# Optimization experiments

Measured on AMD Instinct MI355X. Metric: run time of the kernel, lower is better.

The kernel has to match this reference:

```python
import jax, jax.numpy as jnp
import numpy as np

N, E, F, R, S = 20000, 320000, 64, 8, 10
AVG_NEIGH = 16.0


def setup_inputs() -> dict:
    key = jax.random.key(0)
    ks = jax.random.split(key, 16)
    inp = {
        "vectors": jax.random.normal(ks[0], (E, 3), jnp.float32),
        "node_feats": jax.random.normal(ks[1], (N, F, 4), jnp.float32),  # [N, F, 1(0e)+3(1o)]
        "node_specie": jax.random.randint(ks[2], (N,), 0, S),
        "radial_embedding": jax.random.normal(ks[3], (E, R), jnp.float32),
        "senders": jax.random.randint(ks[4], (E,), 0, N),
        "receivers": jax.random.randint(ks[5], (E,), 0, N),
        # residual FullyConnectedTensorProduct(feats, one-hot species 0e) == species-dep. linear per l
        "W_res_s": jax.random.normal(ks[6], (S, F, F), jnp.float32),
        "W_res_v": jax.random.normal(ks[7], (S, F, F), jnp.float32),
        # interaction block: input linear per l
        "W_in_s": jax.random.normal(ks[8], (F, F), jnp.float32),
        "W_in_v": jax.random.normal(ks[9], (F, F), jnp.float32),
        # radial MLP -> 5 CG tensor-product path weights per channel
        "mlp_w1": jax.random.normal(ks[10], (R, 64), jnp.float32),
        "mlp_w2": jax.random.normal(ks[11], (64, 5 * F), jnp.float32) / 8.0,
        # interaction block: output linear per l
        "W_out_s": jax.random.normal(ks[12], (F, F), jnp.float32),
        "W_out_v": jax.random.normal(ks[13], (F, F), jnp.float32),
        # symmetric product basis (correlation 3), species-dependent term weights
        "W_prod_s": jax.random.normal(ks[14], (S, 5, F), jnp.float32) * 0.3,
        "W_prod_v": jax.random.normal(ks[15], (S, 4, F), jnp.float32) * 0.3,
    }
    k2 = jax.random.split(jax.random.key(1), 3)
    inp["W_lin_s"] = jax.random.normal(k2[0], (F, F), jnp.float32)
    inp["W_lin_v"] = jax.random.normal(k2[1], (F, F), jnp.float32)
    inp["W_read"] = jax.random.normal(k2[2], (F, 1), jnp.float32)
    return inp


def _forward(vectors, node_feats, node_specie, radial_embedding, senders, receivers,
             W_res_s, W_res_v, W_in_s, W_in_v, mlp_w1, mlp_w2, W_out_s, W_out_v,
             W_prod_s, W_prod_v, W_lin_s, W_lin_v, W_read):
    inv_sf = 1.0 / jnp.sqrt(jnp.float32(F))
    s = node_feats[..., 0]          # [N,F]   0e channels
    v = node_feats[..., 1:]         # [N,F,3] 1o channels

    # --- residual connection: FCTP(feats, one-hot species 0e attrs) -> species-gated linear per l
    res_s = jnp.einsum('nf,ngf->ng', s, W_res_s[node_specie]) * inv_sf
    res_v = jnp.einsum('nfc,ngf->ngc', v, W_res_v[node_specie]) * inv_sf

    # --- InteractionBlock ---
    h_s = (s @ W_in_s) * inv_sf
    h_v = jnp.einsum('nfc,fg->ngc', v, W_in_v) * inv_sf

    # spherical harmonics up to max_ell=1: Y0 = 1, Y1 = unit edge vector
    r = jnp.sqrt(jnp.sum(vectors * vectors, -1) + 1e-12)
    Y1 = vectors / r[:, None]                                # [E,3]

    # radial MLP produces per-edge weights for the 5 CG paths:
    # (0e x Y0 -> 0e), (1o . Y1 -> 0e), (0e x Y1 -> 1o), (1o x Y0 -> 1o), (1o x Y1 -> 1o, cross)
    w = (jax.nn.silu(radial_embedding @ mlp_w1) @ mlp_w2).reshape(-1, 5, F)  # [E,5,F]

    ss = h_s[senders]                                        # [E,F]
    sv = h_v[senders]                                        # [E,F,3]
    dot = jnp.einsum('efc,ec->ef', sv, Y1)                   # [E,F]
    m_s = w[:, 0] * ss + w[:, 1] * dot                       # [E,F]
    m_v = (w[:, 2] * ss)[:, :, None] * Y1[:, None, :] \
        + w[:, 3][:, :, None] * sv \
        + w[:, 4][:, :, None] * jnp.cross(sv, Y1[:, None, :])  # [E,F,3]

    agg_s = jnp.zeros_like(h_s).at[receivers].add(m_s) / AVG_NEIGH
    agg_v = jnp.zeros_like(h_v).at[receivers].add(m_v) / AVG_NEIGH
    a_s = (agg_s @ W_out_s) * inv_sf
    a_v = jnp.einsum('nfc,fg->ngc', agg_v, W_out_v) * inv_sf

    # --- EquivariantProductBasisBlock: correlation-3 symmetric contraction, species-dependent ---
    vv = jnp.sum(a_v * a_v, -1)                              # [N,F] invariant |v|^2
    Wp = W_prod_s[node_specie]                               # [N,5,F]
    p_s = (Wp[:, 0] * a_s + Wp[:, 1] * a_s ** 2 + Wp[:, 2] * a_s ** 3
           + Wp[:, 3] * vv + Wp[:, 4] * a_s * vv)
    Wv = W_prod_v[node_specie]                               # [N,4,F]
    p_v = (Wv[:, 0] + Wv[:, 1] * a_s + Wv[:, 2] * a_s ** 2 + Wv[:, 3] * vv)[:, :, None] * a_v

    f_s = (p_s @ W_lin_s) * inv_sf + res_s
    f_v = jnp.einsum('nfc,fg->ngc', p_v, W_lin_v) * inv_sf + res_v

    # --- LinearReadoutBlock (output_irreps = 0e), 1 head ---
    node_out = ((f_s @ W_read) * inv_sf)[:, None, :]         # [N, heads=1, 1]
    new_feats = jnp.concatenate([f_s[..., None], f_v], axis=-1)  # [N,F,4]
    return node_out, new_feats


def reference(vectors, node_feats, node_specie, radial_embedding, senders, receivers,
              W_res_s, W_res_v, W_in_s, W_in_v, mlp_w1, mlp_w2, W_out_s, W_out_v,
              W_prod_s, W_prod_v, W_lin_s, W_lin_v, W_read):
    return _forward(vectors, node_feats, node_specie, radial_embedding, senders, receivers,
                    W_res_s, W_res_v, W_in_s, W_in_v, mlp_w1, mlp_w2, W_out_s, W_out_v,
                    W_prod_s, W_prod_v, W_lin_s, W_lin_v, W_read)
```

## Files before the change

kernel.cpp:

```cpp
#include <hip/hip_runtime.h>
#include <math.h>

#define NN 20000
#define NE 320000
#define NF (NN*64)
#define TB 16

__global__ __launch_bounds__(256) void k_transpose_res(
    const float* __restrict__ Ws, const float* __restrict__ Wv,
    float* __restrict__ Wst, float* __restrict__ Wvt)
{
  int i = blockIdx.x*256 + threadIdx.x;
  int spec = i >> 12;
  int g = (i >> 6) & 63;
  int f = i & 63;
  Wst[spec*4096 + f*64 + g] = Ws[i];
  Wvt[spec*4096 + f*64 + g] = Wv[i];
}

__global__ __launch_bounds__(256) void k_hist_rank(const int* __restrict__ receivers,
                                                   int* __restrict__ count,
                                                   int* __restrict__ rank)
{
  int e = blockIdx.x*256 + threadIdx.x;
  rank[e] = atomicAdd(&count[receivers[e]], 1);
}

__global__ __launch_bounds__(256) void k_scan(const int* __restrict__ count,
                                              int* __restrict__ offset)
{
  __shared__ int part[256];
  int t = threadIdx.x;
  const int PER = 79;
  int s = 0;
  for(int i=0;i<PER;++i){ int idx = t*PER+i; if(idx < NN) s += count[idx]; }
  part[t] = s;
  __syncthreads();
  for(int off=1; off<256; off<<=1){
    int v = (t>=off) ? part[t-off] : 0;
    __syncthreads();
    part[t] += v;
    __syncthreads();
  }
  int run = t ? part[t-1] : 0;
  for(int i=0;i<PER;++i){
    int idx = t*PER+i;
    if(idx < NN){ offset[idx] = run; run += count[idx]; }
  }
  if(t==255) offset[NN] = run;
}

__global__ __launch_bounds__(256) void k_scatter(
    const int* __restrict__ senders, const int* __restrict__ receivers,
    const float* __restrict__ vectors, const float* __restrict__ radial,
    const int* __restrict__ offset, const int* __restrict__ rank,
    int* __restrict__ srt_snd, int* __restrict__ srt_rcv,
    float* __restrict__ srt_y, float* __restrict__ srt_rad)
{
  int e = blockIdx.x*256 + threadIdx.x;
  int r = receivers[e];
  int slot = offset[r] + rank[e];
  srt_snd[slot] = senders[e];
  srt_rcv[slot] = r;
  float vx = vectors[e*3], vy = vectors[e*3+1], vz = vectors[e*3+2];
  float rinv = rsqrtf(vx*vx + vy*vy + vz*vz + 1e-12f);
  float4 y4; y4.x = vx*rinv; y4.y = vy*rinv; y4.z = vz*rinv; y4.w = 0.f;
  *(float4*)(srt_y + (size_t)slot*4) = y4;
  float4 ra = *(const float4*)(radial + (size_t)e*8);
  float4 rb = *(const float4*)(radial + (size_t)e*8 + 4);
  *(float4*)(srt_rad + (size_t)slot*8)     = ra;
  *(float4*)(srt_rad + (size_t)slot*8 + 4) = rb;
}

__global__ __launch_bounds__(256) void k_node_pre(
    const float* __restrict__ node_feats, const float* __restrict__ W_in_s,
    const float* __restrict__ W_in_v, float* __restrict__ h)
{
  __shared__ float sh[16][4][64];
  int wave = threadIdx.x >> 6, lane = threadIdx.x & 63;
  int nb = blockIdx.x*16 + wave*4;
  #pragma unroll
  for(int k=0;k<4;++k){
    int nd = wave*4 + k;
    float4 nf = *(const float4*)(node_feats + (size_t)((nb+k)*64 + lane)*4);
    sh[nd][0][lane]=nf.x; sh[nd][1][lane]=nf.y; sh[nd][2][lane]=nf.z; sh[nd][3][lane]=nf.w;
  }
  __syncthreads();
  float as[4]={0,0,0,0}, a0[4]={0,0,0,0}, a1[4]={0,0,0,0}, a2[4]={0,0,0,0};
  for(int f=0; f<64; ++f){
    float ws = W_in_s[f*64+lane], wv = W_in_v[f*64+lane];
    #pragma unroll
    for(int k=0;k<4;++k){
      int nd = wave*4 + k;
      as[k] = fmaf(sh[nd][0][f], ws, as[k]);
      a0[k] = fmaf(sh[nd][1][f], wv, a0[k]);
      a1[k] = fmaf(sh[nd][2][f], wv, a1[k]);
      a2[k] = fmaf(sh[nd][3][f], wv, a2[k]);
    }
  }
  #pragma unroll
  for(int k=0;k<4;++k){
    float4 o4; o4.x = as[k]*0.125f; o4.y = a0[k]*0.125f;
    o4.z = a1[k]*0.125f; o4.w = a2[k]*0.125f;
    *(float4*)(h + (size_t)((nb+k)*64 + lane)*4) = o4;
  }
}

__global__ __launch_bounds__(256) void k_edge(
    const float* __restrict__ srt_y, const float* __restrict__ srt_rad,
    const int* __restrict__ srt_snd, const int* __restrict__ srt_rcv,
    const float* __restrict__ mlp_w1, const float* __restrict__ mlp_w2,
    const float* __restrict__ h, float* __restrict__ agg)
{
  __shared__ int   sndS[4][TB];
  __shared__ int   rcvS[4][TB];
  __shared__ float yS[4][4*TB];
  __shared__ float rad[4][8*TB];
  __shared__ float hid[4][TB][64];
  int wave = threadIdx.x >> 6, lane = threadIdx.x & 63;
  int e0 = (blockIdx.x*4 + wave)*TB;

  if(lane < TB){
    sndS[wave][lane] = srt_snd[e0 + lane];
    rcvS[wave][lane] = srt_rcv[e0 + lane];
  }
  yS[wave][lane]     = srt_y[(size_t)e0*4 + lane];
  rad[wave][lane]    = srt_rad[(size_t)e0*8 + lane];
  rad[wave][64+lane] = srt_rad[(size_t)e0*8 + 64 + lane];
  float wl[8];
  #pragma unroll
  for(int r=0;r<8;++r) wl[r] = mlp_w1[r*64+lane];

  #pragma unroll
  for(int t=0;t<TB;++t){
    float acc = 0.f;
    #pragma unroll
    for(int r=0;r<8;++r) acc = fmaf(rad[wave][t*8+r], wl[r], acc);
    hid[wave][t][lane] = acc / (1.f + __expf(-acc));
  }

  float w[5][TB];
  #pragma unroll
  for(int j=0;j<5;++j)
    #pragma unroll
    for(int t=0;t<TB;++t) w[j][t] = 0.f;
  for(int hh=0; hh<64; hh+=2){
    float b0[5], b1[5];
    #pragma unroll
    for(int j=0;j<5;++j){
      b0[j] = mlp_w2[hh*320     + j*64 + lane];
      b1[j] = mlp_w2[(hh+1)*320 + j*64 + lane];
    }
    #pragma unroll
    for(int t=0;t<TB;++t){
      float2 hb = *(const float2*)&hid[wave][t][hh];
      #pragma unroll
      for(int j=0;j<5;++j) w[j][t] = fmaf(hb.x, b0[j], fmaf(hb.y, b1[j], w[j][t]));
    }
  }

  float4 hv[4];
  #pragma unroll
  for(int p=0;p<4;++p)
    hv[p] = *(const float4*)(h + (size_t)(sndS[wave][p]*64 + lane)*4);

  float as_=0.f, av0=0.f, av1=0.f, av2=0.f;
  int cur = rcvS[wave][0];
  #pragma unroll
  for(int t=0;t<TB;++t){
    float4 hc = hv[t&3];
    if(t+4 < TB)
      hv[t&3] = *(const float4*)(h + (size_t)(sndS[wave][t+4]*64 + lane)*4);
    int rcv = rcvS[wave][t];
    if(rcv != cur){
      size_t ro = (size_t)(cur*64 + lane)*4;
      atomicAdd(&agg[ro],   as_);
      atomicAdd(&agg[ro+1], av0);
      atomicAdd(&agg[ro+2], av1);
      atomicAdd(&agg[ro+3], av2);
      as_=0.f; av0=0.f; av1=0.f; av2=0.f;
      cur = rcv;
    }
    float y0=yS[wave][t*4], y1=yS[wave][t*4+1], y2=yS[wave][t*4+2];
    float ss=hc.x, sv0=hc.y, sv1=hc.z, sv2=hc.w;
    float dot = sv0*y0 + sv1*y1 + sv2*y2;
    as_ += w[0][t]*ss + w[1][t]*dot;
    float w2s = w[2][t]*ss, w3t = w[3][t], w4t = w[4][t];
    av0 += w2s*y0 + w3t*sv0 + w4t*(sv1*y2 - sv2*y1);
    av1 += w2s*y1 + w3t*sv1 + w4t*(sv2*y0 - sv0*y2);
    av2 += w2s*y2 + w3t*sv2 + w4t*(sv0*y1 - sv1*y0);
  }
  size_t ro = (size_t)(cur*64 + lane)*4;
  atomicAdd(&agg[ro],   as_);
  atomicAdd(&agg[ro+1], av0);
  atomicAdd(&agg[ro+2], av1);
  atomicAdd(&agg[ro+3], av2);
}

__global__ __launch_bounds__(256) void k_node_post(
  const float* __restrict__ node_feats, const int* __restrict__ specie,
  const float* __restrict__ agg,
  const float* __restrict__ Wrst, const float* __restrict__ Wrvt,
  const float* __restrict__ W_out_s, const float* __restrict__ W_out_v,
  const float* __restrict__ W_prod_s, const float* __restrict__ W_prod_v,
  const float* __restrict__ W_lin_s, const float* __restrict__ W_lin_v,
  const float* __restrict__ W_read, float* __restrict__ out_node,
  float* __restrict__ out_feats)
{
  __shared__ float shA[16][4][64];
  __shared__ float shS[16][4][64];
  int wave = threadIdx.x >> 6, lane = threadIdx.x & 63;
  int nb = blockIdx.x*16 + wave*4;
  #pragma unroll
  for(int k=0;k<4;++k){
    int nd = wave*4 + k;
    float4 ag = *(const float4*)(agg + (size_t)((nb+k)*64 + lane)*4);
    shA[nd][0][lane] = ag.x * (1.f/16.f);
    shA[nd][1][lane] = ag.y * (1.f/16.f);
    shA[nd][2][lane] = ag.z * (1.f/16.f);
    shA[nd][3][lane] = ag.w * (1.f/16.f);
    float4 nf = *(const float4*)(node_feats + (size_t)((nb+k)*64 + lane)*4);
    shS[nd][0][lane]=nf.x; shS[nd][1][lane]=nf.y; shS[nd][2][lane]=nf.z; shS[nd][3][lane]=nf.w;
  }
  int spec[4];
  #pragma unroll
  for(int k=0;k<4;++k) spec[k] = specie[nb+k];
  __syncthreads();
  float a_s[4]={0,0,0,0}, a0[4]={0,0,0,0}, a1[4]={0,0,0,0}, a2[4]={0,0,0,0};
  float r_s[4]={0,0,0,0}, r0[4]={0,0,0,0}, r1[4]={0,0,0,0}, r2[4]={0,0,0,0};
  for(int f=0; f<64; ++f){
    float wos = W_out_s[f*64+lane], wov = W_out_v[f*64+lane];
    #pragma unroll
    for(int k=0;k<4;++k){
      int nd = wave*4 + k;
      a_s[k] = fmaf(shA[nd][0][f], wos, a_s[k]);
      a0[k]  = fmaf(shA[nd][1][f], wov, a0[k]);
      a1[k]  = fmaf(shA[nd][2][f], wov, a1[k]);
      a2[k]  = fmaf(shA[nd][3][f], wov, a2[k]);
    }
    #pragma unroll
    for(int k=0;k<4;++k){
      int nd = wave*4 + k;
      float wrs = Wrst[spec[k]*4096 + f*64 + lane];
      float wrv = Wrvt[spec[k]*4096 + f*64 + lane];
      r_s[k] = fmaf(shS[nd][0][f], wrs, r_s[k]);
      r0[k]  = fmaf(shS[nd][1][f], wrv, r0[k]);
      r1[k]  = fmaf(shS[nd][2][f], wrv, r1[k]);
      r2[k]  = fmaf(shS[nd][3][f], wrv, r2[k]);
    }
  }
  __syncthreads();
  #pragma unroll
  for(int k=0;k<4;++k){
    int nd = wave*4 + k;
    float A_s = a_s[k]*0.125f, A0 = a0[k]*0.125f, A1 = a1[k]*0.125f, A2 = a2[k]*0.125f;
    float vv = A0*A0 + A1*A1 + A2*A2;
    float as2 = A_s*A_s;
    const float* Wp = W_prod_s + spec[k]*320;
    float p_s = Wp[lane]*A_s + Wp[64+lane]*as2 + Wp[128+lane]*as2*A_s
              + Wp[192+lane]*vv + Wp[256+lane]*A_s*vv;
    const float* Wq = W_prod_v + spec[k]*256;
    float coef = Wq[lane] + Wq[64+lane]*A_s + Wq[128+lane]*as2 + Wq[192+lane]*vv;
    shS[nd][0][lane] = p_s;
    shS[nd][1][lane] = coef*A0;
    shS[nd][2][lane] = coef*A1;
    shS[nd][3][lane] = coef*A2;
  }
  __syncthreads();
  float lfs[4]={0,0,0,0}, lf0[4]={0,0,0,0}, lf1[4]={0,0,0,0}, lf2[4]={0,0,0,0};
  for(int f=0; f<64; ++f){
    float wls = W_lin_s[f*64+lane], wlv = W_lin_v[f*64+lane];
    #pragma unroll
    for(int k=0;k<4;++k){
      int nd = wave*4 + k;
      lfs[k] = fmaf(shS[nd][0][f], wls, lfs[k]);
      lf0[k] = fmaf(shS[nd][1][f], wlv, lf0[k]);
      lf1[k] = fmaf(shS[nd][2][f], wlv, lf1[k]);
      lf2[k] = fmaf(shS[nd][3][f], wlv, lf2[k]);
    }
  }
  float wr = W_read[lane];
  #pragma unroll
  for(int k=0;k<4;++k){
    int n = nb + k;
    float FS = lfs[k]*0.125f + r_s[k]*0.125f;
    float F0 = lf0[k]*0.125f + r0[k]*0.125f;
    float F1 = lf1[k]*0.125f + r1[k]*0.125f;
    float F2 = lf2[k]*0.125f + r2[k]*0.125f;
    float x = FS * wr;
    #pragma unroll
    for(int off=32; off; off>>=1) x += __shfl_down(x, off);
    if(lane==0) out_node[n] = x*0.125f;
    float4 o4; o4.x=FS; o4.y=F0; o4.z=F1; o4.w=F2;
    *(float4*)(out_feats + (size_t)(n*64+lane)*4) = o4;
  }
}

extern "C" void kernel_launch(void* const* d_in, const int* in_sizes, int n_in,
                              void* d_out, int out_size, void* d_ws, size_t ws_size,
                              hipStream_t stream) {
  const float* vectors    = (const float*)d_in[0];
  const float* node_feats = (const float*)d_in[1];
  const int*   node_specie= (const int*)  d_in[2];
  const float* radial     = (const float*)d_in[3];
  const int*   senders    = (const int*)  d_in[4];
  const int*   receivers  = (const int*)  d_in[5];
  const float* W_res_s    = (const float*)d_in[6];
  const float* W_res_v    = (const float*)d_in[7];
  const float* W_in_s     = (const float*)d_in[8];
  const float* W_in_v     = (const float*)d_in[9];
  const float* mlp_w1     = (const float*)d_in[10];
  const float* mlp_w2     = (const float*)d_in[11];
  const float* W_out_s    = (const float*)d_in[12];
  const float* W_out_v    = (const float*)d_in[13];
  const float* W_prod_s   = (const float*)d_in[14];
  const float* W_prod_v   = (const float*)d_in[15];
  const float* W_lin_s    = (const float*)d_in[16];
  const float* W_lin_v    = (const float*)d_in[17];
  const float* W_read     = (const float*)d_in[18];

  float* ws   = (float*)d_ws;
  float* h    = ws;
  float* agg  = ws + 4*(size_t)NF;
  float* Wrst = ws + 8*(size_t)NF;
  float* Wrvt = Wrst + 40960;
  float* srt_rad = Wrvt + 40960;
  float* srt_y   = srt_rad + 8*(size_t)NE;
  int*   srt_snd = (int*)(srt_y + 4*(size_t)NE);
  int*   srt_rcv = srt_snd + NE;
  int*   rank    = srt_rcv + NE;
  int*   offset  = rank + NE;
  int*   count   = offset + NN + 1;

  hipMemsetAsync(agg,   0, (size_t)4*NF*sizeof(float), stream);
  hipMemsetAsync(count, 0, (size_t)NN*sizeof(int), stream);
  k_transpose_res<<<160, 256, 0, stream>>>(W_res_s, W_res_v, Wrst, Wrvt);
  k_hist_rank<<<NE/256, 256, 0, stream>>>(receivers, count, rank);
  k_scan     <<<1,      256, 0, stream>>>(count, offset);
  k_scatter  <<<NE/256, 256, 0, stream>>>(senders, receivers, vectors, radial,
                                          offset, rank, srt_snd, srt_rcv, srt_y, srt_rad);
  k_node_pre<<<NN/16, 256, 0, stream>>>(node_feats, W_in_s, W_in_v, h);
  k_edge<<<NE/(4*TB), 256, 0, stream>>>(srt_y, srt_rad, srt_snd, srt_rcv,
                                        mlp_w1, mlp_w2, h, agg);
  k_node_post<<<NN/16, 256, 0, stream>>>(node_feats, node_specie, agg,
                                         Wrst, Wrvt, W_out_s, W_out_v,
                                         W_prod_s, W_prod_v, W_lin_s, W_lin_v,
                                         W_read, (float*)d_out, (float*)d_out + NN);
}
```

Before: 536.7 us.

## Pack sorted edge data into 64-byte records and use packed FMA for radial MLP

The scatter kernel now writes each sorted edge as one 16-float record (unit vector, sender, radial features, receiver). The edge kernel loads that record with a single coalesced float4 per lane, replacing four separate arrays and their loads. The hid shared buffer is transposed so the 64x320 MLP layer can use packed two-wide FMAs over pairs of edges. The agg buffer also moves to a planar per-node layout, so atomics and the k_node_post loads touch contiguous 64-lane runs; the cost is a padded record that writes extra bytes in the scatter pass.

```diff
diff --git a/kernel.cpp b/kernel.cpp
--- a/kernel.cpp
+++ b/kernel.cpp
@@ -5,6 +5,16 @@
 #define NE 320000
 #define NF (NN*64)
 #define TB 16
+
+typedef float v2f __attribute__((ext_vector_type(2)));
+
+#if __has_builtin(__builtin_elementwise_fma)
+#define PKFMA(a,b,c) __builtin_elementwise_fma(a,b,c)
+#else
+static __device__ __forceinline__ v2f PKFMA(v2f a, v2f b, v2f c){
+  v2f r; r.x = fmaf(a.x,b.x,c.x); r.y = fmaf(a.y,b.y,c.y); return r;
+}
+#endif
 
 __global__ __launch_bounds__(256) void k_transpose_res(
     const float* __restrict__ Ws, const float* __restrict__ Wv,
@@ -54,22 +64,22 @@
     const int* __restrict__ senders, const int* __restrict__ receivers,
     const float* __restrict__ vectors, const float* __restrict__ radial,
     const int* __restrict__ offset, const int* __restrict__ rank,
-    int* __restrict__ srt_snd, int* __restrict__ srt_rcv,
-    float* __restrict__ srt_y, float* __restrict__ srt_rad)
+    float* __restrict__ rec)
 {
   int e = blockIdx.x*256 + threadIdx.x;
   int r = receivers[e];
   int slot = offset[r] + rank[e];
-  srt_snd[slot] = senders[e];
-  srt_rcv[slot] = r;
   float vx = vectors[e*3], vy = vectors[e*3+1], vz = vectors[e*3+2];
   float rinv = rsqrtf(vx*vx + vy*vy + vz*vz + 1e-12f);
-  float4 y4; y4.x = vx*rinv; y4.y = vy*rinv; y4.z = vz*rinv; y4.w = 0.f;
-  *(float4*)(srt_y + (size_t)slot*4) = y4;
   float4 ra = *(const float4*)(radial + (size_t)e*8);
   float4 rb = *(const float4*)(radial + (size_t)e*8 + 4);
-  *(float4*)(srt_rad + (size_t)slot*8)     = ra;
-  *(float4*)(srt_rad + (size_t)slot*8 + 4) = rb;
+  float* rp = rec + (size_t)slot*16;
+  float4 w0; w0.x = vx*rinv; w0.y = vy*rinv; w0.z = vz*rinv; w0.w = __int_as_float(senders[e]);
+  float4 w3; w3.x = __int_as_float(r); w3.y = 0.f; w3.z = 0.f; w3.w = 0.f;
+  *(float4*)(rp)      = w0;
+  *(float4*)(rp + 4)  = ra;
+  *(float4*)(rp + 8)  = rb;
+  *(float4*)(rp + 12) = w3;
 }
 
 __global__ __launch_bounds__(256) void k_node_pre(
@@ -107,26 +117,17 @@
 }
 
 __global__ __launch_bounds__(256) void k_edge(
-    const float* __restrict__ srt_y, const float* __restrict__ srt_rad,
-    const int* __restrict__ srt_snd, const int* __restrict__ srt_rcv,
+    const float* __restrict__ rec,
     const float* __restrict__ mlp_w1, const float* __restrict__ mlp_w2,
     const float* __restrict__ h, float* __restrict__ agg)
 {
-  __shared__ int   sndS[4][TB];
-  __shared__ int   rcvS[4][TB];
-  __shared__ float yS[4][4*TB];
-  __shared__ float rad[4][8*TB];
-  __shared__ float hid[4][TB][64];
+  __shared__ float recS[4][256];
+  __shared__ float hid[4][64][20];
   int wave = threadIdx.x >> 6, lane = threadIdx.x & 63;
   int e0 = (blockIdx.x*4 + wave)*TB;
 
-  if(lane < TB){
-    sndS[wave][lane] = srt_snd[e0 + lane];
-    rcvS[wave][lane] = srt_rcv[e0 + lane];
-  }
-  yS[wave][lane]     = srt_y[(size_t)e0*4 + lane];
-  rad[wave][lane]    = srt_rad[(size_t)e0*8 + lane];
-  rad[wave][64+lane] = srt_rad[(size_t)e0*8 + 64 + lane];
+  *(float4*)&recS[wave][lane*4] = *(const float4*)(rec + (size_t)e0*16 + lane*4);
+
   float wl[8];
   #pragma unroll
   for(int r=0;r<8;++r) wl[r] = mlp_w1[r*64+lane];
@@ -135,66 +136,73 @@
   for(int t=0;t<TB;++t){
     float acc = 0.f;
     #pragma unroll
-    for(int r=0;r<8;++r) acc = fmaf(rad[wave][t*8+r], wl[r], acc);
-    hid[wave][t][lane] = acc / (1.f + __expf(-acc));
-  }
-
-  float w[5][TB];
+    for(int r=0;r<8;++r) acc = fmaf(recS[wave][t*16+4+r], wl[r], acc);
+    hid[wave][lane][t] = acc / (1.f + __expf(-acc));
+  }
+
+  v2f wv[5][8];
   #pragma unroll
   for(int j=0;j<5;++j)
     #pragma unroll
-    for(int t=0;t<TB;++t) w[j][t] = 0.f;
-  for(int hh=0; hh<64; hh+=2){
-    float b0[5], b1[5];
+    for(int tp=0;tp<8;++tp) wv[j][tp] = (v2f){0.f, 0.f};
+  const float* w2p = mlp_w2 + lane;
+  for(int hh=0; hh<64; ++hh){
+    float b[5];
+    #pragma unroll
+    for(int j=0;j<5;++j) b[j] = w2p[hh*320 + j*64];
+    v2f hv[8];
+    #pragma unroll
+    for(int tp=0;tp<8;++tp) hv[tp] = *(const v2f*)&hid[wave][hh][2*tp];
     #pragma unroll
     for(int j=0;j<5;++j){
-      b0[j] = mlp_w2[hh*320     + j*64 + lane];
-      b1[j] = mlp_w2[(hh+1)*320 + j*64 + lane];
-    }
-    #pragma unroll
-    for(int t=0;t<TB;++t){
-      float2 hb = *(const float2*)&hid[wave][t][hh];
+      v2f bb = {b[j], b[j]};
       #pragma unroll
-      for(int j=0;j<5;++j) w[j][t] = fmaf(hb.x, b0[j], fmaf(hb.y, b1[j], w[j][t]));
-    }
-  }
-
-  float4 hv[4];
-  #pragma unroll
-  for(int p=0;p<4;++p)
-    hv[p] = *(const float4*)(h + (size_t)(sndS[wave][p]*64 + lane)*4);
+      for(int tp=0;tp<8;++tp) wv[j][tp] = PKFMA(bb, hv[tp], wv[j][tp]);
+    }
+  }
+
+  float4 hv4[4];
+  #pragma unroll
+  for(int p=0;p<4;++p){
+    int snd = __float_as_int(recS[wave][p*16+3]);
+    hv4[p] = *(const float4*)(h + (size_t)(snd*64 + lane)*4);
+  }
 
   float as_=0.f, av0=0.f, av1=0.f, av2=0.f;
-  int cur = rcvS[wave][0];
+  int cur = __float_as_int(recS[wave][12]);
   #pragma unroll
   for(int t=0;t<TB;++t){
-    float4 hc = hv[t&3];
-    if(t+4 < TB)
-      hv[t&3] = *(const float4*)(h + (size_t)(sndS[wave][t+4]*64 + lane)*4);
-    int rcv = rcvS[wave][t];
+    float4 hc = hv4[t&3];
+    if(t+4 < TB){
+      int snd = __float_as_int(recS[wave][(t+4)*16+3]);
+      hv4[t&3] = *(const float4*)(h + (size_t)(snd*64 + lane)*4);
+    }
+    int rcv = __float_as_int(recS[wave][t*16+12]);
     if(rcv != cur){
-      size_t ro = (size_t)(cur*64 + lane)*4;
-      atomicAdd(&agg[ro],   as_);
-      atomicAdd(&agg[ro+1], av0);
-      atomicAdd(&agg[ro+2], av1);
-      atomicAdd(&agg[ro+3], av2);
+      size_t ro = (size_t)cur*256 + lane;
+      atomicAdd(&agg[ro],     as_);
+      atomicAdd(&agg[ro+64],  av0);
+      atomicAdd(&agg[ro+128], av1);
+      atomicAdd(&agg[ro+192], av2);
       as_=0.f; av0=0.f; av1=0.f; av2=0.f;
       cur = rcv;
     }
-    float y0=yS[wave][t*4], y1=yS[wave][t*4+1], y2=yS[wave][t*4+2];
+    float y0=recS[wave][t*16], y1=recS[wave][t*16+1], y2=recS[wave][t*16+2];
     float ss=hc.x, sv0=hc.y, sv1=hc.z, sv2=hc.w;
     float dot = sv0*y0 + sv1*y1 + sv2*y2;
-    as_ += w[0][t]*ss + w[1][t]*dot;
-    float w2s = w[2][t]*ss, w3t = w[3][t], w4t = w[4][t];
-    av0 += w2s*y0 + w3t*sv0 + w4t*(sv1*y2 - sv2*y1);
-    av1 += w2s*y1 + w3t*sv1 + w4t*(sv2*y0 - sv0*y2);
-    av2 += w2s*y2 + w3t*sv2 + w4t*(sv0*y1 - sv1*y0);
-  }
-  size_t ro = (size_t)(cur*64 + lane)*4;
-  atomicAdd(&agg[ro],   as_);
-  atomicAdd(&agg[ro+1], av0);
-  atomicAdd(&agg[ro+2], av1);
-  atomicAdd(&agg[ro+3], av2);
+    float wt0 = wv[0][t>>1][t&1], wt1 = wv[1][t>>1][t&1];
+    float wt2 = wv[2][t>>1][t&1], wt3 = wv[3][t>>1][t&1], wt4 = wv[4][t>>1][t&1];
+    as_ += wt0*ss + wt1*dot;
+    float w2s = wt2*ss;
+    av0 += w2s*y0 + wt3*sv0 + wt4*(sv1*y2 - sv2*y1);
+    av1 += w2s*y1 + wt3*sv1 + wt4*(sv2*y0 - sv0*y2);
+    av2 += w2s*y2 + wt3*sv2 + wt4*(sv0*y1 - sv1*y0);
+  }
+  size_t ro = (size_t)cur*256 + lane;
+  atomicAdd(&agg[ro],     as_);
+  atomicAdd(&agg[ro+64],  av0);
+  atomicAdd(&agg[ro+128], av1);
+  atomicAdd(&agg[ro+192], av2);
 }
 
 __global__ __launch_bounds__(256) void k_node_post(
@@ -214,11 +222,11 @@
   #pragma unroll
   for(int k=0;k<4;++k){
     int nd = wave*4 + k;
-    float4 ag = *(const float4*)(agg + (size_t)((nb+k)*64 + lane)*4);
-    shA[nd][0][lane] = ag.x * (1.f/16.f);
-    shA[nd][1][lane] = ag.y * (1.f/16.f);
-    shA[nd][2][lane] = ag.z * (1.f/16.f);
-    shA[nd][3][lane] = ag.w * (1.f/16.f);
+    size_t o = (size_t)(nb+k)*256 + lane;
+    shA[nd][0][lane] = agg[o]      * (1.f/16.f);
+    shA[nd][1][lane] = agg[o+64]   * (1.f/16.f);
+    shA[nd][2][lane] = agg[o+128]  * (1.f/16.f);
+    shA[nd][3][lane] = agg[o+192]  * (1.f/16.f);
     float4 nf = *(const float4*)(node_feats + (size_t)((nb+k)*64 + lane)*4);
     shS[nd][0][lane]=nf.x; shS[nd][1][lane]=nf.y; shS[nd][2][lane]=nf.z; shS[nd][3][lane]=nf.w;
   }
@@ -324,13 +332,10 @@
   float* agg  = ws + 4*(size_t)NF;
   float* Wrst = ws + 8*(size_t)NF;
   float* Wrvt = Wrst + 40960;
-  float* srt_rad = Wrvt + 40960;
-  float* srt_y   = srt_rad + 8*(size_t)NE;
-  int*   srt_snd = (int*)(srt_y + 4*(size_t)NE);
-  int*   srt_rcv = srt_snd + NE;
-  int*   rank    = srt_rcv + NE;
-  int*   offset  = rank + NE;
-  int*   count   = offset + NN + 1;
+  float* rec  = Wrvt + 40960;
+  int*   rank   = (int*)(rec + 16*(size_t)NE);
+  int*   offset = rank + NE;
+  int*   count  = offset + NN + 1;
 
   hipMemsetAsync(agg,   0, (size_t)4*NF*sizeof(float), stream);
   hipMemsetAsync(count, 0, (size_t)NN*sizeof(int), stream);
@@ -338,10 +343,9 @@
   k_hist_rank<<<NE/256, 256, 0, stream>>>(receivers, count, rank);
   k_scan     <<<1,      256, 0, stream>>>(count, offset);
   k_scatter  <<<NE/256, 256, 0, stream>>>(senders, receivers, vectors, radial,
-                                          offset, rank, srt_snd, srt_rcv, srt_y, srt_rad);
+                                          offset, rank, rec);
   k_node_pre<<<NN/16, 256, 0, stream>>>(node_feats, W_in_s, W_in_v, h);
-  k_edge<<<NE/(4*TB), 256, 0, stream>>>(srt_y, srt_rad, srt_snd, srt_rcv,
-                                        mlp_w1, mlp_w2, h, agg);
+  k_edge<<<NE/(4*TB), 256, 0, stream>>>(rec, mlp_w1, mlp_w2, h, agg);
   k_node_post<<<NN/16, 256, 0, stream>>>(node_feats, node_specie, agg,
                                          Wrst, Wrvt, W_out_s, W_out_v,
                                          W_prod_s, W_prod_v, W_lin_s, W_lin_v,
```

Result: faster. 483.8 us (-9.9%).
